# Performance work log

Measured on AMD Instinct MI355X. Metric: run time of the kernel, lower is better.

## Reference

```python
import jax, jax.numpy as jnp
import numpy as np

B, S, D, H = 4, 2048, 1024, 16
DEPTH = D // H


def setup_inputs() -> dict:
    key = jax.random.key(0)
    ks = jax.random.split(key, 11)
    s = 1.0 / np.sqrt(D)
    return {
        "q": jax.random.normal(ks[0], (B, S, D), jnp.float32),
        "k": jax.random.normal(ks[1], (B, S, D), jnp.float32),
        "v": jax.random.normal(ks[2], (B, S, D), jnp.float32),
        "wq": jax.random.normal(ks[3], (D, D), jnp.float32) * s,
        "bq": jnp.zeros((D,), jnp.float32),
        "wk": jax.random.normal(ks[4], (D, D), jnp.float32) * s,
        "bk": jnp.zeros((D,), jnp.float32),
        "wv": jax.random.normal(ks[5], (D, D), jnp.float32) * s,
        "bv": jnp.zeros((D,), jnp.float32),
        "wo": jax.random.normal(ks[6], (D, D), jnp.float32) * s,
        "bo": jnp.zeros((D,), jnp.float32),
    }


def _split_heads(x):
    # [B,S,D] -> [B,H,S,depth]
    b, s, _ = x.shape
    return x.reshape(b, s, H, DEPTH).transpose(0, 2, 1, 3)


def reference(q, k, v, wq, bq, wk, bk, wv, bv, wo, bo):
    qh = _split_heads(q @ wq + bq)
    kh = _split_heads(k @ wk + bk)
    vh = _split_heads(v @ wv + bv)
    scale = 1.0 / jnp.sqrt(jnp.asarray(DEPTH, jnp.float32))
    logits = jnp.einsum("bhsd,bhtd->bhst", qh, kh) * scale  # [B,H,S,S]
    attn = jax.nn.softmax(logits, axis=-1)
    out = jnp.einsum("bhst,bhtd->bhsd", attn, vh)
    out = out.transpose(0, 2, 1, 3).reshape(q.shape[0], -1, D)
    return out @ wo + bo
```

## Files before the change

kernel.cpp:

```cpp
#include <hip/hip_runtime.h>
#include <hip/hip_bf16.h>

#define BATCH 4
#define SEQ   2048
#define DIM   1024
#define NHEAD 16
#define HDIM  64

typedef __bf16    bf16x8 __attribute__((ext_vector_type(8)));
typedef float     f32x16 __attribute__((ext_vector_type(16)));
typedef unsigned  u32;

__device__ __forceinline__ unsigned short f2bfu(float x) {
  union { __hip_bfloat16 b; unsigned short u; } c; c.b = __float2bfloat16(x); return c.u;
}
__device__ __forceinline__ u32 cvtpk(float lo, float hi) {
  u32 r; asm("v_cvt_pk_bf16_f32 %0, %1, %2" : "=v"(r) : "v"(lo), "v"(hi)); return r;
}
__device__ __forceinline__ float max3f(float a, float b, float c) {
  float r; asm("v_max3_f32 %0, %1, %2, %3" : "=v"(r) : "v"(a), "v"(b), "v"(c)); return r;
}
__device__ __forceinline__ int swz4(int row) {
  return ((row & 7) ^ ((row >> 3) & 7)) << 2;
}

#define GLDS16(GP, LP)                                                         \
  __builtin_amdgcn_global_load_lds(                                            \
      (const __attribute__((address_space(1))) void*)(GP),                     \
      (__attribute__((address_space(3))) void*)(LP), 16, 0, 0)

__global__ __launch_bounds__(256)
void wtrans(const float* __restrict__ w0, const float* __restrict__ w1,
            const float* __restrict__ w2,
            __hip_bfloat16* __restrict__ t0, __hip_bfloat16* __restrict__ t1,
            __hip_bfloat16* __restrict__ t2)
{
  __shared__ float T[64][68];
  const int mat  = blockIdx.x >> 8;
  const int tile = blockIdx.x & 255;
  const float* W = mat == 0 ? w0 : (mat == 1 ? w1 : w2);
  __hip_bfloat16* Wt = mat == 0 ? t0 : (mat == 1 ? t1 : t2);
  const int k0 = (tile >> 4) * 64, n0 = (tile & 15) * 64;
  const int tid = threadIdx.x;
  const int r = tid >> 2, cq = (tid & 3) * 16;
  #pragma unroll
  for (int j = 0; j < 4; ++j) {
    const float4 v = *reinterpret_cast<const float4*>(&W[(size_t)(k0 + r) * DIM + n0 + cq + j * 4]);
    T[r][cq + j * 4 + 0] = v.x; T[r][cq + j * 4 + 1] = v.y;
    T[r][cq + j * 4 + 2] = v.z; T[r][cq + j * 4 + 3] = v.w;
  }
  __syncthreads();
  u32 o[8];
  #pragma unroll
  for (int j = 0; j < 8; ++j)
    o[j] = cvtpk(T[cq + 2 * j][r], T[cq + 2 * j + 1][r]);
  *reinterpret_cast<uint4*>(&Wt[(size_t)(n0 + r) * DIM + k0 + cq + 0]) = make_uint4(o[0], o[1], o[2], o[3]);
  *reinterpret_cast<uint4*>(&Wt[(size_t)(n0 + r) * DIM + k0 + cq + 8]) = make_uint4(o[4], o[5], o[6], o[7]);
}

template<typename TIN, typename TOUT, int NSEG>
__global__ __launch_bounds__(256, 2)
void gemm_glds(const TIN* __restrict__ A0, const TIN* __restrict__ A1, const TIN* __restrict__ A2,
               const __hip_bfloat16* __restrict__ W0, const __hip_bfloat16* __restrict__ W1,
               const __hip_bfloat16* __restrict__ W2,
               const float* __restrict__ b0, const float* __restrict__ b1, const float* __restrict__ b2,
               TOUT* __restrict__ C0, TOUT* __restrict__ C1, TOUT* __restrict__ C2)
{
  extern __shared__ char smem[];
  constexpr bool AF32 = (sizeof(TIN) == 4);
  constexpr int ABYTES = 128 * 64 * sizeof(TIN);
  constexpr int K = 1024;

  const int seg = (NSEG == 1) ? 0 : (blockIdx.x >> 9);
  const int idb = (NSEG == 1) ? blockIdx.x : (blockIdx.x & 511);
  const TIN* A = seg == 0 ? A0 : (seg == 1 ? A1 : A2);
  const __hip_bfloat16* Wt = seg == 0 ? W0 : (seg == 1 ? W1 : W2);
  const float* bias = seg == 0 ? b0 : (seg == 1 ? b1 : b2);
  TOUT* C = seg == 0 ? C0 : (seg == 1 ? C1 : C2);

  const int xcd = idb & 7, rr = idb >> 3;
  const int bx = rr & 7, by = xcd + 8 * (rr >> 3);
  const int m0 = by * 128, n0 = bx * 128;

  const int tid = threadIdx.x, lane = tid & 63, w = tid >> 6;
  const int l31 = lane & 31, hi = lane >> 5;
  const int wm = w >> 1, wn = w & 1;

  f32x16 acc[2][2] = {};

  constexpr int NA = AF32 ? 8 : 4;
  const TIN* aptr[NA];
  #pragma unroll
  for (int i = 0; i < NA; ++i) {
    if constexpr (AF32) {
      const int off = (w * 8 + i) * 1024 + lane * 16;
      const int r = off >> 8;
      const int s = (off >> 4) & 15;
      const int e2 = ((r & 7) << 1) | ((r >> 3) & 1);
      aptr[i] = A + (size_t)(m0 + r) * K + (s ^ e2) * 4;
    } else {
      const int off = (w * 4 + i) * 1024 + lane * 16;
      const int r = off >> 7;
      const int s = (off >> 4) & 7;
      aptr[i] = A + (size_t)(m0 + r) * K + (s ^ (r & 7)) * 8;
    }
  }
  const __hip_bfloat16* bptr[4];
  #pragma unroll
  for (int i = 0; i < 4; ++i) {
    const int off = (w * 4 + i) * 1024 + lane * 16;
    const int r = off >> 7;
    const int s = (off >> 4) & 7;
    bptr[i] = Wt + (size_t)(n0 + r) * K + (s ^ (r & 7)) * 8;
  }

  int aoff[4][2], boff[4][2];
  #pragma unroll
  for (int kk = 0; kk < 4; ++kk) {
    #pragma unroll
    for (int mi = 0; mi < 2; ++mi) {
      const int r = wm * 64 + mi * 32 + l31;
      if constexpr (AF32) {
        const int e2 = ((r & 7) << 1) | ((r >> 3) & 1);
        aoff[kk][mi] = r * 256 + (((kk * 4 + hi * 2) ^ e2) << 4);
      } else {
        aoff[kk][mi] = r * 128 + (((kk * 2 + hi) ^ (r & 7)) << 4);
      }
    }
    #pragma unroll
    for (int ni = 0; ni < 2; ++ni) {
      const int c = wn * 64 + ni * 32 + l31;
      boff[kk][ni] = c * 128 + (((kk * 2 + hi) ^ (c & 7)) << 4);
    }
  }

  for (int t = 0; t < 16; ++t) {
    #pragma unroll
    for (int i = 0; i < NA; ++i) {
      GLDS16(aptr[i], smem + (w * NA + i) * 1024);
      aptr[i] += 64;
    }
    #pragma unroll
    for (int i = 0; i < 4; ++i) {
      GLDS16(bptr[i], smem + ABYTES + (w * 4 + i) * 1024);
      bptr[i] += 64;
    }
    __syncthreads();

    #pragma unroll
    for (int kk = 0; kk < 4; ++kk) {
      bf16x8 af[2], bfv[2];
      #pragma unroll
      for (int mi = 0; mi < 2; ++mi) {
        if constexpr (AF32) {
          const float4 f0 = *reinterpret_cast<const float4*>(smem + aoff[kk][mi]);
          const float4 f1 = *reinterpret_cast<const float4*>(smem + (aoff[kk][mi] ^ 16));
          union { u32 u[4]; bf16x8 v; } uu;
          uu.u[0] = cvtpk(f0.x, f0.y); uu.u[1] = cvtpk(f0.z, f0.w);
          uu.u[2] = cvtpk(f1.x, f1.y); uu.u[3] = cvtpk(f1.z, f1.w);
          af[mi] = uu.v;
        } else {
          af[mi] = *reinterpret_cast<const bf16x8*>(smem + aoff[kk][mi]);
        }
      }
      #pragma unroll
      for (int ni = 0; ni < 2; ++ni)
        bfv[ni] = *reinterpret_cast<const bf16x8*>(smem + ABYTES + boff[kk][ni]);
      __builtin_amdgcn_s_setprio(1);
      #pragma unroll
      for (int mi = 0; mi < 2; ++mi)
        #pragma unroll
        for (int ni = 0; ni < 2; ++ni)
          acc[mi][ni] = __builtin_amdgcn_mfma_f32_32x32x16_bf16(af[mi], bfv[ni], acc[mi][ni], 0, 0, 0);
      __builtin_amdgcn_s_setprio(0);
    }
    __syncthreads();
  }

  #pragma unroll
  for (int ni = 0; ni < 2; ++ni) {
    const int col = n0 + wn * 64 + ni * 32 + l31;
    const float bv = bias[col];
    #pragma unroll
    for (int mi = 0; mi < 2; ++mi) {
      #pragma unroll
      for (int g = 0; g < 4; ++g)
        #pragma unroll
        for (int e = 0; e < 4; ++e) {
          const int row = m0 + wm * 64 + mi * 32 + g * 8 + hi * 4 + e;
          const float val = acc[mi][ni][g * 4 + e] + bv;
          if constexpr (sizeof(TOUT) == 2)
            C[(size_t)row * DIM + col] = __float2bfloat16(val);
          else
            C[(size_t)row * DIM + col] = val;
        }
    }
  }
}

__global__ __launch_bounds__(256, 2)
void flash_attn(const __hip_bfloat16* __restrict__ Qb,
                const __hip_bfloat16* __restrict__ Kb,
                const __hip_bfloat16* __restrict__ Vb,
                __hip_bfloat16* __restrict__ Ob)
{
  __shared__ __align__(16) u32 Ks32[2][64][32];
  __shared__ __align__(16) u32 Vt32[2][64][32];

  const int id  = blockIdx.x;
  const int xcd = id & 7;
  const int r_  = id >> 3;
  const int qb  = r_ & 7;
  const int hh  = (r_ >> 3) & 1;
  const int b   = r_ >> 4;
  const int h   = xcd + 8 * hh;

  const int tid = threadIdx.x, lane = tid & 63, wv = tid >> 6;
  const int l31 = lane & 31, hi = lane >> 5;

  const size_t headoff = (size_t)h * HDIM;
  const int q0 = b * SEQ + qb * 256 + wv * 64;

  bf16x8 qf[2][4];
  #pragma unroll
  for (int qh = 0; qh < 2; ++qh)
    #pragma unroll
    for (int dk = 0; dk < 4; ++dk)
      qf[qh][dk] = *reinterpret_cast<const bf16x8*>(
        &Qb[(size_t)(q0 + qh * 32 + l31) * DIM + headoff + dk * 16 + hi * 8]);

  f32x16 accO[2][2] = {};
  float m_run[2] = {-1e30f, -1e30f}, l_run[2] = {0.f, 0.f};

  const int skey = tid >> 2;
  const int sdq  = tid & 3;
  const int vkp  = tid >> 3;
  const int vdb  = tid & 7;
  const size_t kbase = (size_t)b * SEQ * DIM + headoff;

  uint4 kst[2], vst[2];
  auto load_t = [&](int t) {
    const int kb = t * 64;
    const __hip_bfloat16* kp_ = &Kb[kbase + (size_t)(kb + skey) * DIM + sdq * 16];
    kst[0] = *reinterpret_cast<const uint4*>(kp_);
    kst[1] = *reinterpret_cast<const uint4*>(kp_ + 8);
    const __hip_bfloat16* vp_ = &Vb[kbase + (size_t)(kb + vkp * 2) * DIM + vdb * 8];
    vst[0] = *reinterpret_cast<const uint4*>(vp_);
    vst[1] = *reinterpret_cast<const uint4*>(vp_ + DIM);
  };
  auto store_t = [&](int bb) {
    const int sk = swz4(skey);
    *reinterpret_cast<uint4*>(&Ks32[bb][skey][(sdq * 8 + 0) ^ sk]) = kst[0];
    *reinterpret_cast<uint4*>(&Ks32[bb][skey][(sdq * 8 + 4) ^ sk]) = kst[1];
    const unsigned short* a  = (const unsigned short*)&vst[0];
    const unsigned short* bv = (const unsigned short*)&vst[1];
    #pragma unroll
    for (int j = 0; j < 8; ++j) {
      const int row = vdb * 8 + j;
      Vt32[bb][row][vkp ^ swz4(row)] = (u32)a[j] | ((u32)bv[j] << 16);
    }
  };

  load_t(0); store_t(0); __syncthreads();

  const float C1  = 0.125f * 1.44269504f;
  const float L2E = 1.44269504f;

  for (int t = 0; t < SEQ / 64; ++t) {
    const int bb = t & 1;
    if (t < SEQ / 64 - 1) load_t(t + 1);

    f32x16 sacc[2][2] = {};
    __builtin_amdgcn_s_setprio(1);
    #pragma unroll
    for (int kt = 0; kt < 2; ++kt) {
      const int row = kt * 32 + l31;
      const int sk = swz4(row);
      #pragma unroll
      for (int dk = 0; dk < 4; ++dk) {
        bf16x8 kf = *reinterpret_cast<const bf16x8*>(&Ks32[bb][row][(dk * 8 + hi * 4) ^ sk]);
        sacc[0][kt] = __builtin_amdgcn_mfma_f32_32x32x16_bf16(kf, qf[0][dk], sacc[0][kt], 0, 0, 0);
        sacc[1][kt] = __builtin_amdgcn_mfma_f32_32x32x16_bf16(kf, qf[1][dk], sacc[1][kt], 0, 0, 0);
      }
    }
    __builtin_amdgcn_s_setprio(0);

    float pm[2];
    #pragma unroll
    for (int qh = 0; qh < 2; ++qh) {
      float t3[12];
      #pragma unroll
      for (int i = 0; i < 10; ++i) {
        const int i0 = 3 * i, i1 = 3 * i + 1, i2 = 3 * i + 2;
        const float a0 = (i0 < 16) ? sacc[qh][0][i0] : sacc[qh][1][i0 - 16];
        const float a1 = (i1 < 16) ? sacc[qh][0][i1] : sacc[qh][1][i1 - 16];
        const float a2 = (i2 < 16) ? sacc[qh][0][i2] : sacc[qh][1][i2 - 16];
        t3[i] = max3f(a0, a1, a2);
      }
      t3[10] = sacc[qh][1][14]; t3[11] = sacc[qh][1][15];
      const float c0 = max3f(t3[0], t3[1], t3[2]), c1 = max3f(t3[3], t3[4], t3[5]);
      const float c2 = max3f(t3[6], t3[7], t3[8]), c3 = max3f(t3[9], t3[10], t3[11]);
      float mx = fmaxf(max3f(c0, c1, c2), c3);
      mx = fmaxf(mx, __shfl_xor(mx, 32));
      pm[qh] = mx * 0.125f;
    }

    float al[2] = {1.f, 1.f};
    const bool noresc = __all(fmaxf(pm[0] - m_run[0], pm[1] - m_run[1]) <= 8.0f);
    if (!noresc) {
      #pragma unroll
      for (int qh = 0; qh < 2; ++qh) {
        const float mnew = fmaxf(m_run[qh], pm[qh]);
        al[qh] = __builtin_amdgcn_exp2f((m_run[qh] - mnew) * L2E);
        m_run[qh] = mnew;
        accO[qh][0] *= al[qh];
        accO[qh][1] *= al[qh];
      }
    }

    u32 pf[2][4][4];
    #pragma unroll
    for (int qh = 0; qh < 2; ++qh) {
      const float C2 = -m_run[qh] * L2E;
      #pragma unroll
      for (int kt = 0; kt < 2; ++kt)
        #pragma unroll
        for (int r2 = 0; r2 < 16; ++r2)
          sacc[qh][kt][r2] = __builtin_amdgcn_exp2f(fmaf(sacc[qh][kt][r2], C1, C2));
      f32x16 ps = sacc[qh][0] + sacc[qh][1];
      float s8[8];
      #pragma unroll
      for (int i = 0; i < 8; ++i) s8[i] = ps[i] + ps[i + 8];
      float rs = ((s8[0] + s8[1]) + (s8[2] + s8[3])) + ((s8[4] + s8[5]) + (s8[6] + s8[7]));
      rs += __shfl_xor(rs, 32);
      l_run[qh] = fmaf(l_run[qh], al[qh], rs);

#define MAKE_PF(DST, P, B) do {                                            \
      u32 x1 = cvtpk(P[B+0], P[B+1]);                                      \
      u32 y1 = cvtpk(P[B+4], P[B+5]);                                      \
      u32 x2 = cvtpk(P[B+2], P[B+3]);                                      \
      u32 y2 = cvtpk(P[B+6], P[B+7]);                                      \
      auto s1 = __builtin_amdgcn_permlane32_swap(x1, y1, false, false);    \
      auto s2 = __builtin_amdgcn_permlane32_swap(x2, y2, false, false);    \
      DST[0] = (u32)s1[0]; DST[1] = (u32)s2[0];                            \
      DST[2] = (u32)s1[1]; DST[3] = (u32)s2[1];                            \
    } while (0)
      MAKE_PF(pf[qh][0], sacc[qh][0], 0);
      MAKE_PF(pf[qh][1], sacc[qh][0], 8);
      MAKE_PF(pf[qh][2], sacc[qh][1], 0);
      MAKE_PF(pf[qh][3], sacc[qh][1], 8);
#undef MAKE_PF
    }

    __builtin_amdgcn_s_setprio(1);
    #pragma unroll
    for (int dt = 0; dt < 2; ++dt) {
      const int row = dt * 32 + l31;
      const int sk = swz4(row);
      #pragma unroll
      for (int kf = 0; kf < 4; ++kf) {
        bf16x8 vf = *reinterpret_cast<const bf16x8*>(&Vt32[bb][row][(kf * 8 + hi * 4) ^ sk]);
        #pragma unroll
        for (int qh = 0; qh < 2; ++qh) {
          union { u32 u[4]; bf16x8 v; } pu;
          pu.u[0] = pf[qh][kf][0]; pu.u[1] = pf[qh][kf][1];
          pu.u[2] = pf[qh][kf][2]; pu.u[3] = pf[qh][kf][3];
          accO[qh][dt] = __builtin_amdgcn_mfma_f32_32x32x16_bf16(vf, pu.v, accO[qh][dt], 0, 0, 0);
        }
      }
    }
    __builtin_amdgcn_s_setprio(0);

    if (t < SEQ / 64 - 1) store_t(bb ^ 1);
    __syncthreads();
  }

  #pragma unroll
  for (int qh = 0; qh < 2; ++qh) {
    const float inv = 1.f / l_run[qh];
    const size_t rowbase = (size_t)(q0 + qh * 32 + l31) * DIM + headoff;
    #pragma unroll
    for (int dt = 0; dt < 2; ++dt)
      #pragma unroll
      for (int g = 0; g < 4; ++g) {
        ushort4 o;
        o.x = f2bfu(accO[qh][dt][g * 4 + 0] * inv);
        o.y = f2bfu(accO[qh][dt][g * 4 + 1] * inv);
        o.z = f2bfu(accO[qh][dt][g * 4 + 2] * inv);
        o.w = f2bfu(accO[qh][dt][g * 4 + 3] * inv);
        *reinterpret_cast<ushort4*>(&Ob[rowbase + dt * 32 + g * 8 + hi * 4]) = o;
      }
  }
}

extern "C" void kernel_launch(void* const* d_in, const int* in_sizes, int n_in,
                              void* d_out, int out_size, void* d_ws, size_t ws_size,
                              hipStream_t stream)
{
  const float* q  = (const float*)d_in[0];
  const float* k  = (const float*)d_in[1];
  const float* v  = (const float*)d_in[2];
  const float* wq = (const float*)d_in[3];
  const float* bq = (const float*)d_in[4];
  const float* wk = (const float*)d_in[5];
  const float* bk = (const float*)d_in[6];
  const float* wv = (const float*)d_in[7];
  const float* bv = (const float*)d_in[8];
  const float* wo = (const float*)d_in[9];
  const float* bo = (const float*)d_in[10];

  const size_t MN = (size_t)BATCH * SEQ * DIM;
  const size_t KK = (size_t)DIM * DIM;

  __hip_bfloat16* Qb = (__hip_bfloat16*)d_ws;
  __hip_bfloat16* Kb = Qb + MN;
  __hip_bfloat16* Vb = Kb + MN;
  __hip_bfloat16* S3 = Vb + MN;
  __hip_bfloat16* WtQ = S3;
  __hip_bfloat16* WtK = S3 + KK;
  __hip_bfloat16* WtV = S3 + 2 * KK;
  __hip_bfloat16* Ob  = S3;
  __hip_bfloat16* WtO = (__hip_bfloat16*)d_ws;

  wtrans<<<768, 256, 0, stream>>>(wq, wk, wv, WtQ, WtK, WtV);

  gemm_glds<float, __hip_bfloat16, 3><<<1536, 256, 49152, stream>>>(
      q, k, v, WtQ, WtK, WtV, bq, bk, bv, Qb, Kb, Vb);

  flash_attn<<<512, 256, 0, stream>>>(Qb, Kb, Vb, Ob);

  wtrans<<<256, 256, 0, stream>>>(wo, wo, wo, WtO, WtO, WtO);

  gemm_glds<__hip_bfloat16, float, 1><<<512, 256, 32768, stream>>>(
      Ob, Ob, Ob, WtO, WtO, WtO, bo, bo, bo,
      (float*)d_out, (float*)d_out, (float*)d_out);
}
```

Before: 210.5 us.

## Halve per-wave query rows in flash attention and double grid for occupancy

Each wave of the flash attention kernel now handles 32 query rows instead of 64, so a block covers 128 queries and the grid doubles to 1024 blocks. Launch bounds are raised from 2 to 4 blocks per CU, which cuts per-thread register use (accumulators, P fragments) to allow more resident waves. The cost is that every K/V tile loaded into shared memory is reused by half as many queries, doubling total K/V global and LDS traffic per output, and each K fragment read from LDS feeds one MFMA instead of two.

```diff
diff --git a/kernel.cpp b/kernel.cpp
--- a/kernel.cpp
+++ b/kernel.cpp
@@ -198,7 +198,7 @@
   }
 }
 
-__global__ __launch_bounds__(256, 2)
+__global__ __launch_bounds__(256, 4)
 void flash_attn(const __hip_bfloat16* __restrict__ Qb,
                 const __hip_bfloat16* __restrict__ Kb,
                 const __hip_bfloat16* __restrict__ Vb,
@@ -210,27 +210,25 @@
   const int id  = blockIdx.x;
   const int xcd = id & 7;
   const int r_  = id >> 3;
-  const int qb  = r_ & 7;
-  const int hh  = (r_ >> 3) & 1;
-  const int b   = r_ >> 4;
+  const int qb  = r_ & 15;
+  const int hh  = (r_ >> 4) & 1;
+  const int b   = r_ >> 5;
   const int h   = xcd + 8 * hh;
 
   const int tid = threadIdx.x, lane = tid & 63, wv = tid >> 6;
   const int l31 = lane & 31, hi = lane >> 5;
 
   const size_t headoff = (size_t)h * HDIM;
-  const int q0 = b * SEQ + qb * 256 + wv * 64;
-
-  bf16x8 qf[2][4];
-  #pragma unroll
-  for (int qh = 0; qh < 2; ++qh)
-    #pragma unroll
-    for (int dk = 0; dk < 4; ++dk)
-      qf[qh][dk] = *reinterpret_cast<const bf16x8*>(
-        &Qb[(size_t)(q0 + qh * 32 + l31) * DIM + headoff + dk * 16 + hi * 8]);
-
-  f32x16 accO[2][2] = {};
-  float m_run[2] = {-1e30f, -1e30f}, l_run[2] = {0.f, 0.f};
+  const int qrow = b * SEQ + qb * 128 + wv * 32 + l31;
+
+  bf16x8 qf[4];
+  #pragma unroll
+  for (int dk = 0; dk < 4; ++dk)
+    qf[dk] = *reinterpret_cast<const bf16x8*>(
+      &Qb[(size_t)qrow * DIM + headoff + dk * 16 + hi * 8]);
+
+  f32x16 accO[2] = {};
+  float m_run = -1e30f, l_run = 0.f;
 
   const int skey = tid >> 2;
   const int sdq  = tid & 3;
@@ -270,7 +268,7 @@
     const int bb = t & 1;
     if (t < SEQ / 64 - 1) load_t(t + 1);
 
-    f32x16 sacc[2][2] = {};
+    f32x16 sacc[2] = {};
     __builtin_amdgcn_s_setprio(1);
     #pragma unroll
     for (int kt = 0; kt < 2; ++kt) {
@@ -279,62 +277,52 @@
       #pragma unroll
       for (int dk = 0; dk < 4; ++dk) {
         bf16x8 kf = *reinterpret_cast<const bf16x8*>(&Ks32[bb][row][(dk * 8 + hi * 4) ^ sk]);
-        sacc[0][kt] = __builtin_amdgcn_mfma_f32_32x32x16_bf16(kf, qf[0][dk], sacc[0][kt], 0, 0, 0);
-        sacc[1][kt] = __builtin_amdgcn_mfma_f32_32x32x16_bf16(kf, qf[1][dk], sacc[1][kt], 0, 0, 0);
+        sacc[kt] = __builtin_amdgcn_mfma_f32_32x32x16_bf16(kf, qf[dk], sacc[kt], 0, 0, 0);
       }
     }
     __builtin_amdgcn_s_setprio(0);
 
-    float pm[2];
-    #pragma unroll
-    for (int qh = 0; qh < 2; ++qh) {
-      float t3[12];
-      #pragma unroll
-      for (int i = 0; i < 10; ++i) {
-        const int i0 = 3 * i, i1 = 3 * i + 1, i2 = 3 * i + 2;
-        const float a0 = (i0 < 16) ? sacc[qh][0][i0] : sacc[qh][1][i0 - 16];
-        const float a1 = (i1 < 16) ? sacc[qh][0][i1] : sacc[qh][1][i1 - 16];
-        const float a2 = (i2 < 16) ? sacc[qh][0][i2] : sacc[qh][1][i2 - 16];
-        t3[i] = max3f(a0, a1, a2);
-      }
-      t3[10] = sacc[qh][1][14]; t3[11] = sacc[qh][1][15];
-      const float c0 = max3f(t3[0], t3[1], t3[2]), c1 = max3f(t3[3], t3[4], t3[5]);
-      const float c2 = max3f(t3[6], t3[7], t3[8]), c3 = max3f(t3[9], t3[10], t3[11]);
-      float mx = fmaxf(max3f(c0, c1, c2), c3);
-      mx = fmaxf(mx, __shfl_xor(mx, 32));
-      pm[qh] = mx * 0.125f;
-    }
-
-    float al[2] = {1.f, 1.f};
-    const bool noresc = __all(fmaxf(pm[0] - m_run[0], pm[1] - m_run[1]) <= 8.0f);
+    float t3[12];
+    #pragma unroll
+    for (int i = 0; i < 10; ++i) {
+      const int i0 = 3 * i, i1 = 3 * i + 1, i2 = 3 * i + 2;
+      const float a0 = (i0 < 16) ? sacc[0][i0] : sacc[1][i0 - 16];
+      const float a1 = (i1 < 16) ? sacc[0][i1] : sacc[1][i1 - 16];
+      const float a2 = (i2 < 16) ? sacc[0][i2] : sacc[1][i2 - 16];
+      t3[i] = max3f(a0, a1, a2);
+    }
+    t3[10] = sacc[1][14]; t3[11] = sacc[1][15];
+    const float c0 = max3f(t3[0], t3[1], t3[2]), c1 = max3f(t3[3], t3[4], t3[5]);
+    const float c2 = max3f(t3[6], t3[7], t3[8]), c3 = max3f(t3[9], t3[10], t3[11]);
+    float mx = fmaxf(max3f(c0, c1, c2), c3);
+    mx = fmaxf(mx, __shfl_xor(mx, 32));
+    const float pm = mx * 0.125f;
+
+    float al = 1.f;
+    const bool noresc = __all(pm - m_run <= 8.0f);
     if (!noresc) {
-      #pragma unroll
-      for (int qh = 0; qh < 2; ++qh) {
-        const float mnew = fmaxf(m_run[qh], pm[qh]);
-        al[qh] = __builtin_amdgcn_exp2f((m_run[qh] - mnew) * L2E);
-        m_run[qh] = mnew;
-        accO[qh][0] *= al[qh];
-        accO[qh][1] *= al[qh];
-      }
-    }
-
-    u32 pf[2][4][4];
-    #pragma unroll
-    for (int qh = 0; qh < 2; ++qh) {
-      const float C2 = -m_run[qh] * L2E;
-      #pragma unroll
-      for (int kt = 0; kt < 2; ++kt)
-        #pragma unroll
-        for (int r2 = 0; r2 < 16; ++r2)
-          sacc[qh][kt][r2] = __builtin_amdgcn_exp2f(fmaf(sacc[qh][kt][r2], C1, C2));
-      f32x16 ps = sacc[qh][0] + sacc[qh][1];
-      float s8[8];
-      #pragma unroll
-      for (int i = 0; i < 8; ++i) s8[i] = ps[i] + ps[i + 8];
-      float rs = ((s8[0] + s8[1]) + (s8[2] + s8[3])) + ((s8[4] + s8[5]) + (s8[6] + s8[7]));
-      rs += __shfl_xor(rs, 32);
-      l_run[qh] = fmaf(l_run[qh], al[qh], rs);
-
+      const float mnew = fmaxf(m_run, pm);
+      al = __builtin_amdgcn_exp2f((m_run - mnew) * L2E);
+      m_run = mnew;
+      accO[0] *= al;
+      accO[1] *= al;
+    }
+
+    const float C2 = -m_run * L2E;
+    #pragma unroll
+    for (int kt = 0; kt < 2; ++kt)
+      #pragma unroll
+      for (int r2 = 0; r2 < 16; ++r2)
+        sacc[kt][r2] = __builtin_amdgcn_exp2f(fmaf(sacc[kt][r2], C1, C2));
+    f32x16 ps = sacc[0] + sacc[1];
+    float s8[8];
+    #pragma unroll
+    for (int i = 0; i < 8; ++i) s8[i] = ps[i] + ps[i + 8];
+    float rs = ((s8[0] + s8[1]) + (s8[2] + s8[3])) + ((s8[4] + s8[5]) + (s8[6] + s8[7]));
+    rs += __shfl_xor(rs, 32);
+    l_run = fmaf(l_run, al, rs);
+
+    u32 pf[4][4];
 #define MAKE_PF(DST, P, B) do {                                            \
       u32 x1 = cvtpk(P[B+0], P[B+1]);                                      \
       u32 y1 = cvtpk(P[B+4], P[B+5]);                                      \
@@ -345,12 +333,11 @@
       DST[0] = (u32)s1[0]; DST[1] = (u32)s2[0];                            \
       DST[2] = (u32)s1[1]; DST[3] = (u32)s2[1];                            \
     } while (0)
-      MAKE_PF(pf[qh][0], sacc[qh][0], 0);
-      MAKE_PF(pf[qh][1], sacc[qh][0], 8);
-      MAKE_PF(pf[qh][2], sacc[qh][1], 0);
-      MAKE_PF(pf[qh][3], sacc[qh][1], 8);
+    MAKE_PF(pf[0], sacc[0], 0);
+    MAKE_PF(pf[1], sacc[0], 8);
+    MAKE_PF(pf[2], sacc[1], 0);
+    MAKE_PF(pf[3], sacc[1], 8);
 #undef MAKE_PF
-    }
 
     __builtin_amdgcn_s_setprio(1);
     #pragma unroll
@@ -360,13 +347,10 @@
       #pragma unroll
       for (int kf = 0; kf < 4; ++kf) {
         bf16x8 vf = *reinterpret_cast<const bf16x8*>(&Vt32[bb][row][(kf * 8 + hi * 4) ^ sk]);
-        #pragma unroll
-        for (int qh = 0; qh < 2; ++qh) {
-          union { u32 u[4]; bf16x8 v; } pu;
-          pu.u[0] = pf[qh][kf][0]; pu.u[1] = pf[qh][kf][1];
-          pu.u[2] = pf[qh][kf][2]; pu.u[3] = pf[qh][kf][3];
-          accO[qh][dt] = __builtin_amdgcn_mfma_f32_32x32x16_bf16(vf, pu.v, accO[qh][dt], 0, 0, 0);
-        }
+        union { u32 u[4]; bf16x8 v; } pu;
+        pu.u[0] = pf[kf][0]; pu.u[1] = pf[kf][1];
+        pu.u[2] = pf[kf][2]; pu.u[3] = pf[kf][3];
+        accO[dt] = __builtin_amdgcn_mfma_f32_32x32x16_bf16(vf, pu.v, accO[dt], 0, 0, 0);
       }
     }
     __builtin_amdgcn_s_setprio(0);
@@ -375,22 +359,19 @@
     __syncthreads();
   }
 
-  #pragma unroll
-  for (int qh = 0; qh < 2; ++qh) {
-    const float inv = 1.f / l_run[qh];
-    const size_t rowbase = (size_t)(q0 + qh * 32 + l31) * DIM + headoff;
-    #pragma unroll
-    for (int dt = 0; dt < 2; ++dt)
-      #pragma unroll
-      for (int g = 0; g < 4; ++g) {
-        ushort4 o;
-        o.x = f2bfu(accO[qh][dt][g * 4 + 0] * inv);
-        o.y = f2bfu(accO[qh][dt][g * 4 + 1] * inv);
-        o.z = f2bfu(accO[qh][dt][g * 4 + 2] * inv);
-        o.w = f2bfu(accO[qh][dt][g * 4 + 3] * inv);
-        *reinterpret_cast<ushort4*>(&Ob[rowbase + dt * 32 + g * 8 + hi * 4]) = o;
-      }
-  }
+  const float inv = 1.f / l_run;
+  const size_t rowbase = (size_t)qrow * DIM + headoff;
+  #pragma unroll
+  for (int dt = 0; dt < 2; ++dt)
+    #pragma unroll
+    for (int g = 0; g < 4; ++g) {
+      ushort4 o;
+      o.x = f2bfu(accO[dt][g * 4 + 0] * inv);
+      o.y = f2bfu(accO[dt][g * 4 + 1] * inv);
+      o.z = f2bfu(accO[dt][g * 4 + 2] * inv);
+      o.w = f2bfu(accO[dt][g * 4 + 3] * inv);
+      *reinterpret_cast<ushort4*>(&Ob[rowbase + dt * 32 + g * 8 + hi * 4]) = o;
+    }
 }
 
 extern "C" void kernel_launch(void* const* d_in, const int* in_sizes, int n_in,
@@ -427,7 +408,7 @@
   gemm_glds<float, __hip_bfloat16, 3><<<1536, 256, 49152, stream>>>(
       q, k, v, WtQ, WtK, WtV, bq, bk, bv, Qb, Kb, Vb);
 
-  flash_attn<<<512, 256, 0, stream>>>(Qb, Kb, Vb, Ob);
+  flash_attn<<<1024, 256, 0, stream>>>(Qb, Kb, Vb, Ob);
 
   wtrans<<<256, 256, 0, stream>>>(wo, wo, wo, WtO, WtO, WtO);
 
```

After: 228.2 us. 8.4% more time.
